# Performance work log

Hardware: AMD Instinct MI355X
Metric: run time of the kernel (lower is better)

The kernel has to match this reference:

```python
import jax, jax.numpy as jnp
import numpy as np

EPS = 1e-8


def setup_inputs() -> dict:
    key = jax.random.key(0)
    k1, k2 = jax.random.split(key)
    a = jax.random.normal(k1, (1, 256, 128, 128), dtype=jnp.float32)
    b = jax.random.normal(k2, (1, 256, 128, 128), dtype=jnp.float32)
    return {"a": a, "b": b}


def reference(a, b):
    # a: [n, c, h, w] rendered feats; b: [n, c, h2, w2] style feats (n == 1)
    n, c, h, w = a.shape
    a_flat = a.reshape(n, c, -1)            # [n, c, hw]
    b_flat = b.reshape(n, c, -1)            # [n, c, h2w2]

    # argmin_cos_distance: channel-wise L2 normalize, cosine distance, argmin
    b_norm = jnp.sqrt((b_flat * b_flat).sum(1, keepdims=True) + EPS)
    b_n = b_flat / (b_norm + EPS)
    a_norm = jnp.sqrt((a_flat * a_flat).sum(1, keepdims=True) + EPS)
    a_n = a_flat / (a_norm + EPS)
    d_mat = 1.0 - jnp.einsum('ncp,ncq->npq', a_n, b_n)   # [n, hw, h2w2]
    z_best = jnp.argmin(d_mat, axis=2)                    # [n, hw]

    # nn_feat_replace: gather matched (unnormalized) style features
    idx = jnp.broadcast_to(z_best[:, None, :], b_flat.shape)
    target = jnp.take_along_axis(b_flat, idx, axis=2).reshape(n, c, h, w)

    # cos_loss(a, target): cosine distance over channel dim, mean over pixels
    an = jnp.sqrt((a * a).sum(1, keepdims=True))
    tn = jnp.sqrt((target * target).sum(1, keepdims=True))
    cossim = ((a / (an + EPS)) * (target / (tn + EPS))).sum(1)  # [n, h, w]
    return (1.0 - cossim).mean()
```

## Files before the change

kernel.cpp:

```cpp
#include <hip/hip_runtime.h>
#include <stdint.h>

#define EPS 1e-8f

constexpr int HW = 16384;
constexpr int BM = 128;
constexpr int NG = 2048;

typedef __attribute__((ext_vector_type(4))) float floatx4;
typedef __attribute__((ext_vector_type(4))) int   intx4;
typedef __attribute__((ext_vector_type(8))) int   intx8;
typedef unsigned char u8;
typedef unsigned int u32;
typedef unsigned long long u64;

typedef const __attribute__((address_space(1))) u32 gas_u32;
typedef __attribute__((address_space(3))) u32 las_u32;
__device__ inline void stage16(const void* g, void* l) {
    __builtin_amdgcn_global_load_lds((gas_u32*)g, (las_u32*)l, 16, 0, 0);
}

__device__ inline u32 pk4(float x0, float x1, float x2, float x3) {
    int t = __builtin_amdgcn_cvt_pk_fp8_f32(x0, x1, 0, false);
    t = __builtin_amdgcn_cvt_pk_fp8_f32(x2, x3, t, true);
    return (u32)t;
}

__device__ inline float getc(const float4& f, int j) {
    return (j == 0) ? f.x : (j == 1) ? f.y : (j == 2) ? f.z : f.w;
}

__global__ __launch_bounds__(512) void prep_kernel(const float* __restrict__ a,
                                                   const float* __restrict__ b,
                                                   float* __restrict__ sumsq_a,
                                                   float* __restrict__ sumsq_b,
                                                   u8* __restrict__ aF, u8* __restrict__ bF,
                                                   u64* __restrict__ packed,
                                                   float* __restrict__ out) {
    __shared__ float red[64][33];
    __shared__ float invb_sh[32];
    const int tid = threadIdx.x;
    const int pg = tid & 7, tc = tid >> 3;
    const int p0 = blockIdx.x * 32, pb = pg * 4;
    const int c0 = tc * 4;
    const u32 fb = (u32)((c0 >> 7) * 2048 + ((c0 >> 4) & 1) * 1024 + (c0 & 15));
    const u32 qr16 = (u32)(((c0 >> 5) & 3) * 16);

    if (blockIdx.x < 32) packed[(size_t)blockIdx.x * 512 + tid] = 0ull;
    if (blockIdx.x == 0 && tid == 0) *out = 0.f;

    float4 bv[4], av[4];
    #pragma unroll
    for (int i = 0; i < 4; ++i)
        bv[i] = *(const float4*)&b[(size_t)(c0 + i) * HW + p0 + pb];
    #pragma unroll
    for (int i = 0; i < 4; ++i)
        av[i] = *(const float4*)&a[(size_t)(c0 + i) * HW + p0 + pb];

    float s0 = 0.f, s1 = 0.f, s2 = 0.f, s3 = 0.f;
    #pragma unroll
    for (int i = 0; i < 4; ++i) {
        s0 += bv[i].x * bv[i].x; s1 += bv[i].y * bv[i].y;
        s2 += bv[i].z * bv[i].z; s3 += bv[i].w * bv[i].w;
    }
    red[tc][pb] = s0; red[tc][pb + 1] = s1; red[tc][pb + 2] = s2; red[tc][pb + 3] = s3;
    __syncthreads();
    if (tid < 32) {
        float B = 0.f;
        #pragma unroll
        for (int j = 0; j < 64; ++j) B += red[j][tid];
        sumsq_b[p0 + tid] = B;
        invb_sh[tid] = 1.0f / (sqrtf(B + EPS) + EPS);
    }
    __syncthreads();

    #pragma unroll
    for (int j = 0; j < 4; ++j) {
        const int p = p0 + pb + j;
        const float inv = invb_sh[pb + j];
        u32 wv = pk4(getc(bv[0], j) * inv, getc(bv[1], j) * inv,
                     getc(bv[2], j) * inv, getc(bv[3], j) * inv);
        *(u32*)(bF + ((size_t)(p >> 4) << 12) + fb + (qr16 + (u32)(p & 15)) * 16) = wv;
    }

    s0 = s1 = s2 = s3 = 0.f;
    #pragma unroll
    for (int i = 0; i < 4; ++i) {
        s0 += av[i].x * av[i].x; s1 += av[i].y * av[i].y;
        s2 += av[i].z * av[i].z; s3 += av[i].w * av[i].w;
    }
    red[tc][pb] = s0; red[tc][pb + 1] = s1; red[tc][pb + 2] = s2; red[tc][pb + 3] = s3;
    #pragma unroll
    for (int j = 0; j < 4; ++j) {
        const int p = p0 + pb + j;
        u32 wv = pk4(getc(av[0], j), getc(av[1], j), getc(av[2], j), getc(av[3], j));
        *(u32*)(aF + ((size_t)(p >> 4) << 12) + fb + (qr16 + (u32)(p & 15)) * 16) = wv;
    }
    __syncthreads();
    if (tid < 32) {
        float A = 0.f;
        #pragma unroll
        for (int j = 0; j < 64; ++j) A += red[j][tid];
        sumsq_a[p0 + tid] = A;
    }
}

#define MFMA1(A_, B_, C_) __builtin_amdgcn_mfma_scale_f32_16x16x128_f8f6f4( \
        (A_), (B_), (C_), 0, 0, 0, SCL, 0, SCL)

#define LDB(off_) __builtin_shufflevector(                                  \
        *(const intx4*)(Lb + (off_)), *(const intx4*)(Lb + (off_) + 1024),  \
        0, 1, 2, 3, 4, 5, 6, 7)

#define MFMA_QT(acc_, buf_) do {                                            \
    const u8* Lb = &sB[buf_][(u32)(wn * 2) * 4096u + (u32)lane * 16u];      \
    intx8 Bk0n0 = LDB(0);                                                   \
    intx8 Bk0n1 = LDB(4096);                                                \
    __builtin_amdgcn_s_setprio(1);                                          \
    acc_[0][0] = MFMA1(Afr[0][0], Bk0n0, C64);                              \
    acc_[1][0] = MFMA1(Afr[1][0], Bk0n0, C64);                              \
    acc_[0][1] = MFMA1(Afr[0][0], Bk0n1, C64);                              \
    acc_[1][1] = MFMA1(Afr[1][0], Bk0n1, C64);                              \
    __builtin_amdgcn_s_setprio(0);                                          \
    intx8 Bk1n0 = LDB(2048);                                                \
    intx8 Bk1n1 = LDB(4096 + 2048);                                         \
    __builtin_amdgcn_s_setprio(1);                                          \
    acc_[0][0] = MFMA1(Afr[0][1], Bk1n0, acc_[0][0]);                       \
    acc_[1][0] = MFMA1(Afr[1][1], Bk1n0, acc_[1][0]);                       \
    acc_[0][1] = MFMA1(Afr[0][1], Bk1n1, acc_[0][1]);                       \
    acc_[1][1] = MFMA1(Afr[1][1], Bk1n1, acc_[1][1]);                       \
    __builtin_amdgcn_s_setprio(0);                                          \
} while (0)

#define ARGMAX_QT(acc_, qt_) do {                                           \
    const u32 qb_ = q0 + (u32)(qt_) * 64u;                                  \
    _Pragma("unroll")                                                       \
    for (int mi = 0; mi < 2; ++mi) {                                        \
        _Pragma("unroll")                                                   \
        for (int ni = 0; ni < 2; ++ni) {                                    \
            const u32 qc_ = qb_ + (u32)(ni * 16);                           \
            _Pragma("unroll")                                               \
            for (int r = 0; r < 4; ++r) {                                   \
                float v_ = acc_[mi][ni][r];                                 \
                bool gt_ = v_ > bestv[mi][r];                               \
                bestv[mi][r] = gt_ ? v_ : bestv[mi][r];                     \
                bestq[mi][r] = gt_ ? qc_ : bestq[mi][r];                    \
            }                                                               \
        }                                                                   \
    }                                                                       \
} while (0)

#define STAGE(buf_, qt_) do {                                               \
    const u8* gs_ = gQ + (u32)(qt_) * 16384u + so;                          \
    stage16(gs_, &sB[buf_][wso]);                                           \
    stage16(gs_ + 1024, &sB[buf_][wso + 1024]);                             \
} while (0)

__global__ __launch_bounds__(512, 2) void gemm_argmax(const u8* __restrict__ aF,
                                                      const u8* __restrict__ bF,
                                                      u64* __restrict__ packed) {
    __shared__ u8 sB[2][16384];
    const int tid = threadIdx.x;
    const int w = tid >> 6, lane = tid & 63;
    const int q4 = lane >> 4, r15 = lane & 15;
    const int wm = w >> 1, wn = w & 1;

    const u32 bid = blockIdx.x;
    const u32 ng = bid & 7;
    const u32 mt = bid >> 3;
    const int p0 = (int)mt * BM;

    const u8* gA = aF + (((size_t)(mt * 8 + wm * 2)) << 12) + (u32)lane * 16;
    intx8 Afr[2][2];
    #pragma unroll
    for (int mi = 0; mi < 2; ++mi)
        #pragma unroll
        for (int kb = 0; kb < 2; ++kb)
            Afr[mi][kb] = __builtin_shufflevector(
                *(const intx4*)(gA + (u32)(mi * 4096 + kb * 2048)),
                *(const intx4*)(gA + (u32)(mi * 4096 + kb * 2048 + 1024)),
                0, 1, 2, 3, 4, 5, 6, 7);

    const u8* gQ = bF + ((size_t)ng << 19);
    const u32 so  = (u32)w * 2048u + (u32)lane * 16u;
    const u32 wso = (u32)w * 2048u;

    float bestv[2][4];
    u32   bestq[2][4];
    #pragma unroll
    for (int mi = 0; mi < 2; ++mi)
        #pragma unroll
        for (int r = 0; r < 4; ++r) { bestv[mi][r] = -3.4e38f; bestq[mi][r] = 0; }

    const u32 q0 = ng * 2048 + wn * 32 + (u32)r15;
    const floatx4 C64 = {64.f, 64.f, 64.f, 64.f};
    const int SCL = 0x7F7F7F7F;

    floatx4 accA[2][2], accB[2][2];

    STAGE(0, 0);
    __syncthreads();

    STAGE(1, 1);
    MFMA_QT(accA, 0);
    __syncthreads();

    STAGE(0, 2);
    MFMA_QT(accB, 1);
    ARGMAX_QT(accA, 0);
    __syncthreads();

    for (int i = 1; i <= 14; ++i) {
        const int qtA = 2 * i;
        STAGE(1, qtA + 1);
        MFMA_QT(accA, 0);
        ARGMAX_QT(accB, qtA - 1);
        __syncthreads();

        STAGE(0, qtA + 2);
        MFMA_QT(accB, 1);
        ARGMAX_QT(accA, qtA);
        __syncthreads();
    }

    STAGE(1, 31);
    MFMA_QT(accA, 0);
    ARGMAX_QT(accB, 29);
    __syncthreads();

    MFMA_QT(accB, 1);
    ARGMAX_QT(accA, 30);
    ARGMAX_QT(accB, 31);

    #pragma unroll
    for (int mi = 0; mi < 2; ++mi)
        #pragma unroll
        for (int r = 0; r < 4; ++r) {
            u64 pk = ((u64)__float_as_uint(bestv[mi][r]) << 32)
                   | (u64)(0xFFFFFFFFu - bestq[mi][r]);
            #pragma unroll
            for (int d = 1; d < 16; d <<= 1) {
                u64 o = __shfl_xor((unsigned long long)pk, d);
                pk = o > pk ? o : pk;
            }
            if (r15 == 0)
                atomicMax(&packed[p0 + wm * 32 + mi * 16 + q4 * 4 + r], pk);
        }
}

__global__ void loss_kernel(const u64* __restrict__ packed,
                            const float* __restrict__ sumsq_a, const float* __restrict__ sumsq_b,
                            float* __restrict__ out) {
    int p = blockIdx.x * 256 + threadIdx.x;
    u64 pk = packed[p];
    float s = __uint_as_float((u32)(pk >> 32)) - 64.0f;
    u32 q = 0xFFFFFFFFu - (u32)(pk & 0xFFFFFFFFull);
    float A = sumsq_a[p], B = sumsq_b[q];
    float dot = s * (sqrtf(B + EPS) + EPS);
    float cossim = dot / ((sqrtf(A) + EPS) * (sqrtf(B) + EPS));
    float v = (1.0f - cossim) * (1.0f / (float)HW);
    #pragma unroll
    for (int d = 1; d < 64; d <<= 1) v += __shfl_xor(v, d);
    if ((threadIdx.x & 63) == 0) atomicAdd(out, v);
}

extern "C" void kernel_launch(void* const* d_in, const int* in_sizes, int n_in,
                              void* d_out, int out_size, void* d_ws, size_t ws_size,
                              hipStream_t stream) {
    const float* a = (const float*)d_in[0];
    const float* b = (const float*)d_in[1];
    float* out = (float*)d_out;
    char* ws = (char*)d_ws;

    u8*    aF      = (u8*)ws;
    u8*    bF      = (u8*)(ws + (size_t)4 * 1024 * 1024);
    float* sumsq_a = (float*)(ws + (size_t)8 * 1024 * 1024);
    float* sumsq_b = sumsq_a + HW;
    u64*   packed  = (u64*)(sumsq_b + HW);

    prep_kernel<<<dim3(HW / 32), 512, 0, stream>>>(a, b, sumsq_a, sumsq_b, aF, bF, packed, out);
    gemm_argmax<<<dim3((HW / BM) * (HW / NG)), 512, 0, stream>>>(aF, bF, packed);
    loss_kernel<<<dim3(HW / 256), 256, 0, stream>>>(packed, sumsq_a, sumsq_b, out);
}
```

Measured before the change: 174.4 us.

## Use 4-wave blocks with larger per-wave tiles and triple-buffered B staging

The GEMM-argmax kernel moves from 512-thread blocks to 256-thread blocks. Each wave now holds four A fragments instead of two, so every B fragment loaded from LDS feeds twice as many MFMAs. The double-buffered B pipeline becomes a three-slot ring with an explicit vmcnt wait and one barrier per tile. The prep kernel is also reshaped to 16-pixel blocks with a two-level shared-memory reduction. The cost is higher register pressure from the larger A and accumulator sets, and 48KB of LDS per block.

After: 211.4 us. 21.2% more time.

```diff
diff --git a/kernel.cpp b/kernel.cpp
--- a/kernel.cpp
+++ b/kernel.cpp
@@ -30,23 +30,25 @@
     return (j == 0) ? f.x : (j == 1) ? f.y : (j == 2) ? f.z : f.w;
 }
 
-__global__ __launch_bounds__(512) void prep_kernel(const float* __restrict__ a,
+__global__ __launch_bounds__(256) void prep_kernel(const float* __restrict__ a,
                                                    const float* __restrict__ b,
                                                    float* __restrict__ sumsq_a,
                                                    float* __restrict__ sumsq_b,
                                                    u8* __restrict__ aF, u8* __restrict__ bF,
                                                    u64* __restrict__ packed,
                                                    float* __restrict__ out) {
-    __shared__ float red[64][33];
-    __shared__ float invb_sh[32];
+    __shared__ float red[64][17];
+    __shared__ float p2[8][17];
+    __shared__ float invb_sh[16];
     const int tid = threadIdx.x;
-    const int pg = tid & 7, tc = tid >> 3;
-    const int p0 = blockIdx.x * 32, pb = pg * 4;
+    const int pg = tid & 3, tc = tid >> 2;
+    const int p0 = blockIdx.x * 16, pb = pg * 4;
     const int c0 = tc * 4;
     const u32 fb = (u32)((c0 >> 7) * 2048 + ((c0 >> 4) & 1) * 1024 + (c0 & 15));
     const u32 qr16 = (u32)(((c0 >> 5) & 3) * 16);
-
-    if (blockIdx.x < 32) packed[(size_t)blockIdx.x * 512 + tid] = 0ull;
+    const int px = tid & 15, oct = tid >> 4;
+
+    if (tid < 16) packed[(size_t)blockIdx.x * 16 + tid] = 0ull;
     if (blockIdx.x == 0 && tid == 0) *out = 0.f;
 
     float4 bv[4], av[4];
@@ -65,10 +67,17 @@
     }
     red[tc][pb] = s0; red[tc][pb + 1] = s1; red[tc][pb + 2] = s2; red[tc][pb + 3] = s3;
     __syncthreads();
-    if (tid < 32) {
+    if (tid < 128) {
+        float s = 0.f;
+        #pragma unroll
+        for (int j = 0; j < 8; ++j) s += red[oct * 8 + j][px];
+        p2[oct][px] = s;
+    }
+    __syncthreads();
+    if (tid < 16) {
         float B = 0.f;
         #pragma unroll
-        for (int j = 0; j < 64; ++j) B += red[j][tid];
+        for (int j = 0; j < 8; ++j) B += p2[j][tid];
         sumsq_b[p0 + tid] = B;
         invb_sh[tid] = 1.0f / (sqrtf(B + EPS) + EPS);
     }
@@ -89,6 +98,7 @@
         s0 += av[i].x * av[i].x; s1 += av[i].y * av[i].y;
         s2 += av[i].z * av[i].z; s3 += av[i].w * av[i].w;
     }
+    __syncthreads();
     red[tc][pb] = s0; red[tc][pb + 1] = s1; red[tc][pb + 2] = s2; red[tc][pb + 3] = s3;
     #pragma unroll
     for (int j = 0; j < 4; ++j) {
@@ -97,10 +107,17 @@
         *(u32*)(aF + ((size_t)(p >> 4) << 12) + fb + (qr16 + (u32)(p & 15)) * 16) = wv;
     }
     __syncthreads();
-    if (tid < 32) {
+    if (tid < 128) {
+        float s = 0.f;
+        #pragma unroll
+        for (int j = 0; j < 8; ++j) s += red[oct * 8 + j][px];
+        p2[oct][px] = s;
+    }
+    __syncthreads();
+    if (tid < 16) {
         float A = 0.f;
         #pragma unroll
-        for (int j = 0; j < 64; ++j) A += red[j][tid];
+        for (int j = 0; j < 8; ++j) A += p2[j][tid];
         sumsq_a[p0 + tid] = A;
     }
 }
@@ -112,54 +129,58 @@
         *(const intx4*)(Lb + (off_)), *(const intx4*)(Lb + (off_) + 1024),  \
         0, 1, 2, 3, 4, 5, 6, 7)
 
-#define MFMA_QT(acc_, buf_) do {                                            \
-    const u8* Lb = &sB[buf_][(u32)(wn * 2) * 4096u + (u32)lane * 16u];      \
+#define STAGE(slot_, qt_) do {                                              \
+    const u8* gs_ = gQ + (u32)(qt_) * 16384u + so;                          \
+    u8* ls_ = sB0 + (u32)(slot_) * 16384u + wso;                            \
+    stage16(gs_,        ls_);                                               \
+    stage16(gs_ + 1024, ls_ + 1024);                                        \
+    stage16(gs_ + 2048, ls_ + 2048);                                        \
+    stage16(gs_ + 3072, ls_ + 3072);                                        \
+} while (0)
+
+#define COMPUTE_QT(sc_, qc_) do {                                           \
+    const u8* Lb = sB0 + (u32)(sc_) * 16384u                                \
+                 + (u32)(wn * 2) * 4096u + (u32)lane * 16u;                 \
+    floatx4 acc[4][2];                                                      \
     intx8 Bk0n0 = LDB(0);                                                   \
     intx8 Bk0n1 = LDB(4096);                                                \
     __builtin_amdgcn_s_setprio(1);                                          \
-    acc_[0][0] = MFMA1(Afr[0][0], Bk0n0, C64);                              \
-    acc_[1][0] = MFMA1(Afr[1][0], Bk0n0, C64);                              \
-    acc_[0][1] = MFMA1(Afr[0][0], Bk0n1, C64);                              \
-    acc_[1][1] = MFMA1(Afr[1][0], Bk0n1, C64);                              \
+    _Pragma("unroll")                                                       \
+    for (int mi = 0; mi < 4; ++mi) {                                        \
+        acc[mi][0] = MFMA1(Afr[mi][0], Bk0n0, C64);                         \
+        acc[mi][1] = MFMA1(Afr[mi][0], Bk0n1, C64);                         \
+    }                                                                       \
     __builtin_amdgcn_s_setprio(0);                                          \
     intx8 Bk1n0 = LDB(2048);                                                \
     intx8 Bk1n1 = LDB(4096 + 2048);                                         \
     __builtin_amdgcn_s_setprio(1);                                          \
-    acc_[0][0] = MFMA1(Afr[0][1], Bk1n0, acc_[0][0]);                       \
-    acc_[1][0] = MFMA1(Afr[1][1], Bk1n0, acc_[1][0]);                       \
-    acc_[0][1] = MFMA1(Afr[0][1], Bk1n1, acc_[0][1]);                       \
-    acc_[1][1] = MFMA1(Afr[1][1], Bk1n1, acc_[1][1]);                       \
+    _Pragma("unroll")                                                       \
+    for (int mi = 0; mi < 4; ++mi) {                                        \
+        acc[mi][0] = MFMA1(Afr[mi][1], Bk1n0, acc[mi][0]);                  \
+        acc[mi][1] = MFMA1(Afr[mi][1], Bk1n1, acc[mi][1]);                  \
+    }                                                                       \
     __builtin_amdgcn_s_setprio(0);                                          \
-} while (0)
-
-#define ARGMAX_QT(acc_, qt_) do {                                           \
-    const u32 qb_ = q0 + (u32)(qt_) * 64u;                                  \
     _Pragma("unroll")                                                       \
-    for (int mi = 0; mi < 2; ++mi) {                                        \
+    for (int mi = 0; mi < 4; ++mi) {                                        \
         _Pragma("unroll")                                                   \
         for (int ni = 0; ni < 2; ++ni) {                                    \
-            const u32 qc_ = qb_ + (u32)(ni * 16);                           \
+            const u32 qn_ = (qc_) + (u32)(ni * 16);                         \
             _Pragma("unroll")                                               \
             for (int r = 0; r < 4; ++r) {                                   \
-                float v_ = acc_[mi][ni][r];                                 \
+                float v_ = acc[mi][ni][r];                                  \
                 bool gt_ = v_ > bestv[mi][r];                               \
                 bestv[mi][r] = gt_ ? v_ : bestv[mi][r];                     \
-                bestq[mi][r] = gt_ ? qc_ : bestq[mi][r];                    \
+                bestq[mi][r] = gt_ ? qn_ : bestq[mi][r];                    \
             }                                                               \
         }                                                                   \
     }                                                                       \
 } while (0)
 
-#define STAGE(buf_, qt_) do {                                               \
-    const u8* gs_ = gQ + (u32)(qt_) * 16384u + so;                          \
-    stage16(gs_, &sB[buf_][wso]);                                           \
-    stage16(gs_ + 1024, &sB[buf_][wso + 1024]);                             \
-} while (0)
-
-__global__ __launch_bounds__(512, 2) void gemm_argmax(const u8* __restrict__ aF,
+__global__ __launch_bounds__(256, 3) void gemm_argmax(const u8* __restrict__ aF,
                                                       const u8* __restrict__ bF,
                                                       u64* __restrict__ packed) {
-    __shared__ u8 sB[2][16384];
+    __shared__ u8 sB[3][16384];
+    u8* sB0 = &sB[0][0];
     const int tid = threadIdx.x;
     const int w = tid >> 6, lane = tid & 63;
     const int q4 = lane >> 4, r15 = lane & 15;
@@ -170,10 +191,10 @@
     const u32 mt = bid >> 3;
     const int p0 = (int)mt * BM;
 
-    const u8* gA = aF + (((size_t)(mt * 8 + wm * 2)) << 12) + (u32)lane * 16;
-    intx8 Afr[2][2];
-    #pragma unroll
-    for (int mi = 0; mi < 2; ++mi)
+    const u8* gA = aF + (((size_t)(mt * 8 + wm * 4)) << 12) + (u32)lane * 16;
+    intx8 Afr[4][2];
+    #pragma unroll
+    for (int mi = 0; mi < 4; ++mi)
         #pragma unroll
         for (int kb = 0; kb < 2; ++kb)
             Afr[mi][kb] = __builtin_shufflevector(
@@ -182,58 +203,43 @@
                 0, 1, 2, 3, 4, 5, 6, 7);
 
     const u8* gQ = bF + ((size_t)ng << 19);
-    const u32 so  = (u32)w * 2048u + (u32)lane * 16u;
-    const u32 wso = (u32)w * 2048u;
-
-    float bestv[2][4];
-    u32   bestq[2][4];
-    #pragma unroll
-    for (int mi = 0; mi < 2; ++mi)
+    const u32 so  = (u32)w * 4096u + (u32)lane * 16u;
+    const u32 wso = (u32)w * 4096u;
+
+    float bestv[4][4];
+    u32   bestq[4][4];
+    #pragma unroll
+    for (int mi = 0; mi < 4; ++mi)
         #pragma unroll
         for (int r = 0; r < 4; ++r) { bestv[mi][r] = -3.4e38f; bestq[mi][r] = 0; }
 
-    const u32 q0 = ng * 2048 + wn * 32 + (u32)r15;
+    u32 qcur = ng * 2048 + wn * 32 + (u32)r15;
     const floatx4 C64 = {64.f, 64.f, 64.f, 64.f};
     const int SCL = 0x7F7F7F7F;
 
-    floatx4 accA[2][2], accB[2][2];
-
     STAGE(0, 0);
-    __syncthreads();
-
     STAGE(1, 1);
-    MFMA_QT(accA, 0);
-    __syncthreads();
-
-    STAGE(0, 2);
-    MFMA_QT(accB, 1);
-    ARGMAX_QT(accA, 0);
-    __syncthreads();
-
-    for (int i = 1; i <= 14; ++i) {
-        const int qtA = 2 * i;
-        STAGE(1, qtA + 1);
-        MFMA_QT(accA, 0);
-        ARGMAX_QT(accB, qtA - 1);
-        __syncthreads();
-
-        STAGE(0, qtA + 2);
-        MFMA_QT(accB, 1);
-        ARGMAX_QT(accA, qtA);
-        __syncthreads();
-    }
-
-    STAGE(1, 31);
-    MFMA_QT(accA, 0);
-    ARGMAX_QT(accB, 29);
-    __syncthreads();
-
-    MFMA_QT(accB, 1);
-    ARGMAX_QT(accA, 30);
-    ARGMAX_QT(accB, 31);
-
-    #pragma unroll
-    for (int mi = 0; mi < 2; ++mi)
+
+    int sc = 0;
+    for (int t = 0; t < 31; ++t) {
+        asm volatile("s_waitcnt vmcnt(4)" ::: "memory");
+        __builtin_amdgcn_sched_barrier(0);
+        __builtin_amdgcn_s_barrier();
+        if (t < 30) {
+            const int s2 = sc == 0 ? 2 : sc - 1;
+            STAGE(s2, t + 2);
+        }
+        COMPUTE_QT(sc, qcur);
+        qcur += 64u;
+        sc = sc == 2 ? 0 : sc + 1;
+    }
+    asm volatile("s_waitcnt vmcnt(0)" ::: "memory");
+    __builtin_amdgcn_sched_barrier(0);
+    __builtin_amdgcn_s_barrier();
+    COMPUTE_QT(sc, qcur);
+
+    #pragma unroll
+    for (int mi = 0; mi < 4; ++mi)
         #pragma unroll
         for (int r = 0; r < 4; ++r) {
             u64 pk = ((u64)__float_as_uint(bestv[mi][r]) << 32)
@@ -244,7 +250,7 @@
                 pk = o > pk ? o : pk;
             }
             if (r15 == 0)
-                atomicMax(&packed[p0 + wm * 32 + mi * 16 + q4 * 4 + r], pk);
+                atomicMax(&packed[p0 + wm * 64 + mi * 16 + q4 * 4 + r], pk);
         }
 }
 
@@ -278,7 +284,7 @@
     float* sumsq_b = sumsq_a + HW;
     u64*   packed  = (u64*)(sumsq_b + HW);
 
-    prep_kernel<<<dim3(HW / 32), 512, 0, stream>>>(a, b, sumsq_a, sumsq_b, aF, bF, packed, out);
-    gemm_argmax<<<dim3((HW / BM) * (HW / NG)), 512, 0, stream>>>(aF, bF, packed);
+    prep_kernel<<<dim3(HW / 16), 256, 0, stream>>>(a, b, sumsq_a, sumsq_b, aF, bF, packed, out);
+    gemm_argmax<<<dim3((HW / BM) * (HW / NG)), 256, 0, stream>>>(aF, bF, packed);
     loss_kernel<<<dim3(HW / 256), 256, 0, stream>>>(packed, sumsq_a, sumsq_b, out);
 }
```
